# Kernel tuning notes

Hardware: AMD Instinct MI355X
Metric: run time of the kernel (lower is better)

## Reference

```python
import jax, jax.numpy as jnp
import numpy as np

# Static configuration (mirrors init_kwargs)
B, C, H, W = 4, 256, 128, 128
S, T = 512, 64          # style_dim, num style tokens
HC, HS = 4, 8           # cross-attn heads, spatial-attn heads
WS, G = 8, 4            # window size, groupnorm groups
SHARPEN = 2.0
EPS = 1e-5


def _ln(x, g, b):
    m = jnp.mean(x, -1, keepdims=True)
    v = jnp.var(x, -1, keepdims=True)
    return (x - m) * jax.lax.rsqrt(v + EPS) * g + b


def _sdpa(q, k, v, scale):
    # q,k,v: [B, nH, L, D]
    s = jnp.einsum('bhqd,bhkd->bhqk', q, k) * scale
    return jnp.einsum('bhqk,bhkd->bhqd', jax.nn.softmax(s, -1), v)


def _heads(t, nh):
    b, l, c = t.shape
    return t.reshape(b, l, nh, c // nh).transpose(0, 2, 1, 3)


def _unheads(t):
    b, nh, l, d = t.shape
    return t.transpose(0, 2, 1, 3).reshape(b, l, nh * d)


def setup_inputs() -> dict:
    key = jax.random.key(0)
    ks = iter(jax.random.split(key, 48))
    def w(shape, s=0.02):
        return jax.random.normal(next(ks), shape, jnp.float32) * s
    return {
        'x': jax.random.normal(next(ks), (B, C, H, W), jnp.float32),
        'style_code': jax.random.normal(next(ks), (B, S), jnp.float32),
        # SpatialSelfAttention params (1x1 convs == linear over channels)
        'qkv_w': w((3 * C, C)), 'spat_proj_w': w((C, C)),
        # CrossAttnAdaGN params
        'gproj_w': w((2 * C, S)),
        'gproj_b': jnp.concatenate([jnp.ones((C,), jnp.float32), jnp.zeros((C,), jnp.float32)]),
        'tokens_basis': w((T, C)),
        'sproj_w': w((C, S)), 'sproj_b': jnp.zeros((C,), jnp.float32),
        'pos_w1': w((C, 2)), 'pos_b1': jnp.zeros((C,), jnp.float32),
        'pos_w2': w((C, C)), 'pos_b2': jnp.zeros((C,), jnp.float32),
        'q_w': w((C, C)), 'q_b': jnp.zeros((C,), jnp.float32),
        'k_w': w((C, C)), 'k_b': jnp.zeros((C,), jnp.float32),
        'v_w': w((C, C)), 'v_b': jnp.zeros((C,), jnp.float32),
        'o_w': w((C, C)), 'o_b': jnp.zeros((C,), jnp.float32),
        'ffn_w1': w((2 * C, C)), 'ffn_b1': jnp.zeros((2 * C,), jnp.float32),
        'ffn_w2': w((C, 2 * C)), 'ffn_b2': jnp.zeros((C,), jnp.float32),
        'tn_g': jnp.ones((C,), jnp.float32), 'tn_b': jnp.zeros((C,), jnp.float32),
        'qn_g': jnp.ones((C,), jnp.float32), 'qn_b': jnp.zeros((C,), jnp.float32),
        'fn_g': jnp.ones((C,), jnp.float32), 'fn_b': jnp.zeros((C,), jnp.float32),
        'gamma': w((1, C, 1, 1), 0.1),
    }


def reference(x, style_code, qkv_w, spat_proj_w, gproj_w, gproj_b, tokens_basis,
              sproj_w, sproj_b, pos_w1, pos_b1, pos_w2, pos_b2,
              q_w, q_b, k_w, k_b, v_w, v_b, o_w, o_b,
              ffn_w1, ffn_b1, ffn_w2, ffn_b2,
              tn_g, tn_b, qn_g, qn_b, fn_g, fn_b, gamma):
    b = x.shape[0]
    hw = H * W
    # ---------- CrossAttnAdaGN style modulation ----------
    xg = x.reshape(b, G, C // G, H, W)
    mu = jnp.mean(xg, (2, 3, 4), keepdims=True)
    var = jnp.var(xg, (2, 3, 4), keepdims=True)
    normalized = ((xg - mu) * jax.lax.rsqrt(var + EPS)).reshape(b, C, H, W)
    gp = style_code @ gproj_w.T + gproj_b           # [B, 2C]
    scale = gp[:, :C, None, None]
    shift = gp[:, C:, None, None]
    style_tokens = tokens_basis[None] + (style_code @ sproj_w.T + sproj_b)[:, None]  # [B,T,C]
    style_tokens = _ln(style_tokens, tn_g, tn_b)
    gy = jnp.linspace(-1.0, 1.0, H)
    gx = jnp.linspace(-1.0, 1.0, W)
    grid_y, grid_x = jnp.meshgrid(gy, gx, indexing='ij')
    pos = jnp.stack([grid_x, grid_y], -1).reshape(hw, 2)                 # [HW,2]
    pos_emb = jax.nn.silu(pos @ pos_w1.T + pos_b1) @ pos_w2.T + pos_b2   # [HW,C]
    tok = normalized.transpose(0, 2, 3, 1).reshape(b, hw, C)
    q_in = _ln(tok + pos_emb[None], qn_g, qn_b)
    q = _heads(q_in @ q_w.T + q_b, HC)                 # [B,HC,HW,hd]
    k = _heads(style_tokens @ k_w.T + k_b, HC)         # [B,HC,T,hd]
    v = _heads(style_tokens @ v_w.T + v_b, HC)
    hd = C // HC
    sc = _unheads(_sdpa(q, k, v, SHARPEN / jnp.sqrt(jnp.float32(hd))))   # [B,HW,C]
    sc = sc @ o_w.T + o_b
    sc = sc + jax.nn.silu(_ln(sc, fn_g, fn_b) @ ffn_w1.T + ffn_b1) @ ffn_w2.T + ffn_b2
    sc_sp = sc.transpose(0, 2, 1).reshape(b, C, H, W)
    adagn = normalized * scale + shift + sc_sp * gamma
    h = x + adagn  # gate = 1.0, residual style modulation
    # ---------- shifted-window self-attention ----------
    sh = WS // 2
    xr = jnp.roll(h, (-sh, -sh), (2, 3))
    qkv = jnp.einsum('oi,bihw->bohw', qkv_w, xr)
    qs, ks_, vs = jnp.split(qkv, 3, axis=1)
    def win(t):  # [B,C,H,W] -> [B*nWin, WS*WS, C]
        return t.reshape(b, C, H // WS, WS, W // WS, WS).transpose(0, 2, 4, 3, 5, 1).reshape(-1, WS * WS, C)
    hd2 = C // HS
    qh = _heads(win(qs), HS)
    kh = _heads(win(ks_), HS)
    vh = _heads(win(vs), HS)
    out = _unheads(_sdpa(qh, kh, vh, 1.0 / jnp.sqrt(jnp.float32(hd2))))
    out = out.reshape(b, H // WS, W // WS, WS, WS, C).transpose(0, 5, 1, 3, 2, 4).reshape(b, C, H, W)
    out = jnp.roll(out, (sh, sh), (2, 3))
    out = jnp.einsum('oi,bihw->bohw', spat_proj_w, out)
    return h + out
```

## Files before the change

### kernel.cpp

```cpp
#include <hip/hip_runtime.h>
#include <stdint.h>

#define DEV __device__ __forceinline__

typedef unsigned short u16;
typedef unsigned int u32;
typedef __attribute__((ext_vector_type(8))) __bf16 bf16x8;
typedef __attribute__((ext_vector_type(4))) float f32x4;

DEV u16 f2b(float f) {
  u32 u = __float_as_uint(f);
  u32 r = (u + 0x7FFFu + ((u >> 16) & 1u)) >> 16;
  return (u16)r;
}
DEV float b2f(u16 u) { return __uint_as_float(((u32)u) << 16); }
DEV void up2(u32 u, float& a, float& b) {
  a = __uint_as_float(u << 16);
  b = __uint_as_float(u & 0xffff0000u);
}
DEV void up8(uint4 t, float* d) {
  up2(t.x, d[0], d[1]); up2(t.y, d[2], d[3]);
  up2(t.z, d[4], d[5]); up2(t.w, d[6], d[7]);
}
DEV float silu_f(float v) { return v / (1.0f + __expf(-v)); }

DEV float redmax16(float v) {
  v = fmaxf(v, __shfl_xor(v, 1));
  v = fmaxf(v, __shfl_xor(v, 2));
  v = fmaxf(v, __shfl_xor(v, 4));
  v = fmaxf(v, __shfl_xor(v, 8));
  return v;
}
DEV float redsum16(float v) {
  v += __shfl_xor(v, 1);
  v += __shfl_xor(v, 2);
  v += __shfl_xor(v, 4);
  v += __shfl_xor(v, 8);
  return v;
}

DEV int wperm(int p) {
  int y = p >> 7, x = p & 127;
  return ((((y >> 3) << 4) + (x >> 3)) << 6) + ((y & 7) << 3) + (x & 7);
}

DEV void gload16(const u16* g, u16* l) {
  __builtin_amdgcn_global_load_lds(
      (const __attribute__((address_space(1))) uint32_t*)(g),
      (__attribute__((address_space(3))) uint32_t*)(l), 16, 0, 0);
}

struct WConv {
  const float* s0; const float* s1; const float* s2; const float* s3;
  const float* s4; const float* s5; const float* s6;
  u16* d0; u16* d1; u16* d2; u16* d3; u16* d4; u16* d5; u16* d6;
};
__global__ void k_conv_all(WConv wc) {
  int i = blockIdx.x * 256 + threadIdx.x;
  if (i >= 180224) return;
  const float* sp[7] = {wc.s0, wc.s1, wc.s2, wc.s3, wc.s4, wc.s5, wc.s6};
  u16* dp[7] = {wc.d0, wc.d1, wc.d2, wc.d3, wc.d4, wc.d5, wc.d6};
  const int n4[7] = {16384, 16384, 32768, 32768, 49152, 16384, 16384};
  int rem = i, seg = 0;
#pragma unroll
  for (int s = 0; s < 7; ++s) {
    if (rem < n4[s]) { seg = s; break; }
    rem -= n4[s];
  }
  float4 v = ((const float4*)sp[seg])[rem];
  u16 t[4] = {f2b(v.x), f2b(v.y), f2b(v.z), f2b(v.w)};
  *(uint2*)(dp[seg] + (rem << 2)) = *(uint2*)t;
}

DEV void breduce2(float& a, float& b, float* red, int tid) {
#pragma unroll
  for (int off = 32; off > 0; off >>= 1) {
    a += __shfl_down(a, off);
    b += __shfl_down(b, off);
  }
  int lane = tid & 63, wv = tid >> 6;
  if (lane == 0) { red[wv * 2] = a; red[wv * 2 + 1] = b; }
  __syncthreads();
  a = red[0] + red[2] + red[4] + red[6];
  b = red[1] + red[3] + red[5] + red[7];
}

template <int XB>
__global__ void k_gn_partial(const float* __restrict__ x, float* __restrict__ partials,
                             u16* __restrict__ xb) {
  __shared__ float red[8];
  int chunk = blockIdx.x;
  size_t base4 = ((size_t)chunk) << 12;
  const float4* x4 = (const float4*)x;
  float a = 0.f, b = 0.f;
#pragma unroll 4
  for (int i = 0; i < 16; ++i) {
    size_t idx = base4 + (i << 8) + threadIdx.x;
    float4 v = x4[idx];
    a += v.x + v.y + v.z + v.w;
    b += v.x * v.x + v.y * v.y + v.z * v.z + v.w * v.w;
    if (XB) {
      u16 t[4] = {f2b(v.x), f2b(v.y), f2b(v.z), f2b(v.w)};
      *(uint2*)(xb + (idx << 2)) = *(uint2*)t;
    }
  }
  breduce2(a, b, red, threadIdx.x);
  if (threadIdx.x == 0) { partials[chunk * 2] = a; partials[chunk * 2 + 1] = b; }
}

__global__ void k_gn_final(const float* __restrict__ partials, float* __restrict__ stats) {
  int g = blockIdx.x, lane = threadIdx.x;
  float a = partials[(((g << 6) + lane) << 1)];
  float b = partials[(((g << 6) + lane) << 1) + 1];
#pragma unroll
  for (int off = 32; off > 0; off >>= 1) {
    a += __shfl_down(a, off);
    b += __shfl_down(b, off);
  }
  if (lane == 0) {
    float mean = a * (1.f / 1048576.f);
    float var = b * (1.f / 1048576.f) - mean * mean;
    stats[g << 1] = mean;
    stats[(g << 1) + 1] = rsqrtf(var + 1e-5f);
  }
}

__global__ void k_style(const float* __restrict__ sc, const float* __restrict__ gw,
                        const float* __restrict__ gb, const float* __restrict__ sw,
                        const float* __restrict__ sb, float* __restrict__ gp,
                        float* __restrict__ stok) {
  __shared__ float row[512];
  int b = blockIdx.y, part = blockIdx.x, tid = threadIdx.x;
  row[tid] = sc[(b << 9) + tid];
  row[tid + 256] = sc[(b << 9) + tid + 256];
  __syncthreads();
  if (part < 2) {
    int o = (part << 8) + tid;
    float s = gb[o];
    const float* wr = gw + ((size_t)o << 9);
#pragma unroll 8
    for (int j = 0; j < 512; ++j) s += row[j] * wr[j];
    gp[(b << 9) + o] = s;
  } else {
    float s = sb[tid];
    const float* wr = sw + ((size_t)tid << 9);
#pragma unroll 8
    for (int j = 0; j < 512; ++j) s += row[j] * wr[j];
    stok[(b << 8) + tid] = s;
  }
}

__global__ void k_styk(const float* __restrict__ tb, const float* __restrict__ stok,
                       const float* __restrict__ g, const float* __restrict__ bt,
                       float* __restrict__ styk) {
  __shared__ float red[8];
  int r = blockIdx.x;
  int b = r >> 6, t = r & 63;
  int c = threadIdx.x;
  float v = tb[(t << 8) + c] + stok[(b << 8) + c];
  float a = v, bb = v * v;
  breduce2(a, bb, red, c);
  float mean = a * (1.f / 256.f);
  float var = bb * (1.f / 256.f) - mean * mean;
  float rs = rsqrtf(var + 1e-5f);
  styk[((size_t)r << 8) + c] = (v - mean) * rs * g[c] + bt[c];
}

__global__ void k_kv(const float* __restrict__ styk, const float* __restrict__ kw,
                     const float* __restrict__ kb, const float* __restrict__ vw,
                     const float* __restrict__ vb, u16* __restrict__ kmat,
                     u16* __restrict__ vmat) {
  __shared__ float srow[256];
  int r = blockIdx.x, c = threadIdx.x;
  srow[c] = styk[((size_t)r << 8) + c];
  __syncthreads();
  float sk = kb[c], sv = vb[c];
  const float* kr = kw + ((size_t)c << 8);
  const float* vr = vw + ((size_t)c << 8);
#pragma unroll 8
  for (int j = 0; j < 256; ++j) { sk += srow[j] * kr[j]; sv += srow[j] * vr[j]; }
  kmat[((size_t)r << 8) + c] = f2b(sk);
  vmat[((size_t)r << 8) + c] = f2b(sv);
}

__global__ void k_posh(const float* __restrict__ w1, const float* __restrict__ b1,
                       u16* __restrict__ posh) {
  int i = blockIdx.x * 256 + threadIdx.x;
  int stride = gridDim.x * 256;
  for (; i < 16384 * 256; i += stride) {
    int p = i >> 8, c = i & 255;
    int y = p >> 7, x = p & 127;
    float gx = -1.f + 2.f * (float)x / 127.f;
    float gy = -1.f + 2.f * (float)y / 127.f;
    float v = gx * w1[c << 1] + gy * w1[(c << 1) + 1] + b1[c];
    posh[i] = f2b(silu_f(v));
  }
}

template <int ACT, int BIAS, int RES, int SPLIT>
__global__ __launch_bounds__(256, 2) void k_gemm2(
    const u16* __restrict__ A, const u16* __restrict__ Bw,
    const float* __restrict__ bias, const u16* __restrict__ res,
    u16* __restrict__ o0, u16* __restrict__ o1, u16* __restrict__ o2,
    int M, int N, int K) {
  __shared__ __align__(16) u16 lds[17408];
  u16* sA = lds;
  u16* sB = lds + 4096;
  const int tid = threadIdx.x;
  const int lane = tid & 63, wv = tid >> 6;
  const int nx = gridDim.x;
  const int L = blockIdx.x + nx * blockIdx.y;
  const int xcd = L & 7;
  const int t = L >> 3;
  const int nblk = t % nx;
  const int mblk = ((t / nx) << 3) + xcd;
  const int m0 = mblk << 7, n0 = nblk << 7;
  const int l15 = lane & 15, lg = lane >> 4;
  const int wr = wv >> 1, wc = wv & 1;

  const int gofs = (((lane & 3) ^ ((lane >> 3) & 3)) << 3);
  const int lrow = lane >> 2;
  const u16* Ag0 = A + (size_t)(m0 + (wv << 5) + lrow) * K + gofs;
  const u16* Ag1 = A + (size_t)(m0 + (wv << 5) + 16 + lrow) * K + gofs;
  const u16* Bg0 = Bw + (size_t)(n0 + (wv << 5) + lrow) * K + gofs;
  const u16* Bg1 = Bw + (size_t)(n0 + (wv << 5) + 16 + lrow) * K + gofs;
  u16* lA0 = sA + (wv << 10);
  u16* lA1 = sA + (wv << 10) + 512;
  u16* lB0 = sB + (wv << 10);
  u16* lB1 = sB + (wv << 10) + 512;

  const int roff = l15 * 32 + (((lg ^ ((l15 >> 1) & 3))) << 3);
  const int abase = (wr << 6) * 32;
  const int bbase = (wc << 6) * 32;

  f32x4 acc[4][4];
  f32x4 zz = {0.f, 0.f, 0.f, 0.f};
#pragma unroll
  for (int mi = 0; mi < 4; ++mi)
#pragma unroll
    for (int ni = 0; ni < 4; ++ni) acc[mi][ni] = zz;

  for (int kt = 0; kt < K; kt += 32) {
    __syncthreads();
    gload16(Ag0 + kt, lA0);
    gload16(Ag1 + kt, lA1);
    gload16(Bg0 + kt, lB0);
    gload16(Bg1 + kt, lB1);
    __syncthreads();
    bf16x8 af[4], bfv[4];
#pragma unroll
    for (int mi = 0; mi < 4; ++mi) af[mi] = *(const bf16x8*)&sA[abase + mi * 512 + roff];
#pragma unroll
    for (int ni = 0; ni < 4; ++ni) bfv[ni] = *(const bf16x8*)&sB[bbase + ni * 512 + roff];
#pragma unroll
    for (int mi = 0; mi < 4; ++mi)
#pragma unroll
      for (int ni = 0; ni < 4; ++ni)
        acc[mi][ni] = __builtin_amdgcn_mfma_f32_16x16x32_bf16(af[mi], bfv[ni], acc[mi][ni], 0, 0, 0);
  }

  float bv[4];
#pragma unroll
  for (int ni = 0; ni < 4; ++ni)
    bv[ni] = BIAS ? bias[n0 + (wc << 6) + (ni << 4) + l15] : 0.0f;
  __syncthreads();
  const int lg4 = lg << 2;
#pragma unroll
  for (int mi = 0; mi < 4; ++mi) {
#pragma unroll
    for (int ni = 0; ni < 4; ++ni) {
#pragma unroll
      for (int r = 0; r < 4; ++r) {
        int row = (wr << 6) + (mi << 4) + lg4 + r;
        int col = (wc << 6) + (ni << 4) + l15;
        float v = acc[mi][ni][r] + bv[ni];
        if (ACT == 1) v = silu_f(v);
        lds[row * 136 + col] = f2b(v);
      }
    }
  }
  __syncthreads();
  u16* obase;
  int cb, ldc;
  if (SPLIT) {
    int sel = n0 >> 8;
    obase = sel == 0 ? o0 : (sel == 1 ? o1 : o2);
    cb = n0 & 255;
    ldc = 256;
  } else {
    obase = o0;
    cb = n0;
    ldc = N;
  }
#pragma unroll
  for (int i = 0; i < 8; ++i) {
    int flat = (i << 8) + tid;
    int row = flat >> 4, c8 = (flat & 15) << 3;
    uint4 vv = *(const uint4*)&lds[row * 136 + c8];
    size_t oi;
    if (SPLIT) {
      int m = m0 + row;
      int orow = (m & ~16383) | wperm(m & 16383);
      oi = (size_t)orow * 256 + cb + c8;
    } else {
      oi = (size_t)(m0 + row) * ldc + cb + c8;
    }
    if (RES) {
      uint4 rr = *(const uint4*)(res + oi);
      float a8[8], r8[8];
      up8(vv, a8);
      up8(rr, r8);
      u16 t8[8];
#pragma unroll
      for (int e = 0; e < 8; ++e) t8[e] = f2b(a8[e] + r8[e]);
      vv = *(const uint4*)t8;
    }
    *(uint4*)(obase + oi) = vv;
  }
}

template <int XB>
__global__ __launch_bounds__(256) void k_tokpe2(
    const float* __restrict__ x, const u16* __restrict__ xb,
    const float* __restrict__ stats, const u16* __restrict__ pe,
    const float* __restrict__ qg, const float* __restrict__ qb2,
    u16* __restrict__ tokq) {
  __shared__ u16 T[256 * 72];
  __shared__ float red[64][8];
  const int tid = threadIdx.x;
  const int p0 = blockIdx.x << 6, b = blockIdx.y;
  {
    const int c = tid;
    const int g = (b << 2) + (c >> 6);
    const float mu = stats[g << 1], rs = stats[(g << 1) + 1];
    const size_t base = (((size_t)(b << 8) + c) << 14) + p0;
#pragma unroll
    for (int j8 = 0; j8 < 8; ++j8) {
      float f[8];
      if (XB) {
        up8(*(const uint4*)(xb + base + (j8 << 3)), f);
      } else {
        float4 v0 = *(const float4*)(x + base + (j8 << 3));
        float4 v1 = *(const float4*)(x + base + (j8 << 3) + 4);
        f[0] = v0.x; f[1] = v0.y; f[2] = v0.z; f[3] = v0.w;
        f[4] = v1.x; f[5] = v1.y; f[6] = v1.z; f[7] = v1.w;
      }
      u16 t8[8];
#pragma unroll
      for (int e = 0; e < 8; ++e) t8[e] = f2b((f[e] - mu) * rs);
      *(uint4*)&T[c * 72 + (j8 << 3)] = *(uint4*)t8;
    }
  }
  __syncthreads();
  const int p = tid & 63, cq = tid >> 6;
  const size_t pebase = (((size_t)(p0 + p)) << 8) + (cq << 6);
  float vbuf[64];
  float a = 0.f, s = 0.f;
#pragma unroll
  for (int q = 0; q < 8; ++q) {
    float pf[8];
    up8(*(const uint4*)(pe + pebase + (q << 3)), pf);
#pragma unroll
    for (int e = 0; e < 8; ++e) {
      int j = (q << 3) + e;
      float v = b2f(T[((cq << 6) + j) * 72 + p]) + pf[e];
      vbuf[j] = v;
      a += v; s += v * v;
    }
  }
  red[p][cq << 1] = a;
  red[p][(cq << 1) + 1] = s;
  __syncthreads();
  float sa = red[p][0] + red[p][2] + red[p][4] + red[p][6];
  float ss = red[p][1] + red[p][3] + red[p][5] + red[p][7];
  float mean = sa * (1.f / 256.f);
  float var = ss * (1.f / 256.f) - mean * mean;
  float rsg = rsqrtf(var + 1e-5f);
  const size_t orow = (((size_t)(b << 14) + p0 + p) << 8) + (cq << 6);
#pragma unroll
  for (int q = 0; q < 8; ++q) {
    u16 t8[8];
#pragma unroll
    for (int e = 0; e < 8; ++e) {
      int j = (q << 3) + e;
      t8[e] = f2b((vbuf[j] - mean) * rsg * qg[(cq << 6) + j] + qb2[(cq << 6) + j]);
    }
    *(uint4*)(tokq + orow + (q << 3)) = *(uint4*)t8;
  }
}

__global__ __launch_bounds__(256) void k_rowln8(const u16* __restrict__ in,
                                                const float* __restrict__ g,
                                                const float* __restrict__ bt,
                                                u16* __restrict__ out) {
  __shared__ float gs[256], bs[256];
  int tid = threadIdx.x;
  gs[tid] = g[tid];
  bs[tid] = bt[tid];
  __syncthreads();
  size_t base = (((size_t)(blockIdx.x << 5) + (tid >> 3)) << 8) + ((tid & 7) << 5);
  float v[32];
#pragma unroll
  for (int q = 0; q < 4; ++q) up8(*(const uint4*)(in + base + (q << 3)), &v[q << 3]);
  float a = 0.f, b = 0.f;
#pragma unroll
  for (int j = 0; j < 32; ++j) { a += v[j]; b += v[j] * v[j]; }
#pragma unroll
  for (int m = 1; m <= 4; m <<= 1) { a += __shfl_xor(a, m); b += __shfl_xor(b, m); }
  float mean = a * (1.f / 256.f);
  float var = b * (1.f / 256.f) - mean * mean;
  float rs = rsqrtf(var + 1e-5f);
  int c0 = (tid & 7) << 5;
#pragma unroll
  for (int q = 0; q < 4; ++q) {
    u16 tmp[8];
#pragma unroll
    for (int e = 0; e < 8; ++e) {
      int j = (q << 3) + e;
      tmp[e] = f2b((v[j] - mean) * rs * gs[c0 + j] + bs[c0 + j]);
    }
    *(uint4*)(out + base + (q << 3)) = *(uint4*)tmp;
  }
}

__global__ __launch_bounds__(256, 2) void k_cross_mfma(
    const u16* __restrict__ qmat, const u16* __restrict__ kmat,
    const u16* __restrict__ vmat, u16* __restrict__ attn_out) {
  __shared__ u16 Kl[64 * 72];
  __shared__ u16 Vt[64 * 72];
  __shared__ u16 Pl[4][64 * 72];
  const int tid = threadIdx.x;
  const int lane = tid & 63, wv = tid >> 6;
  const int l15 = lane & 15, lg = lane >> 4;
  const int b = blockIdx.z, h = blockIdx.y;
  const int q0 = blockIdx.x << 8;
  for (int c = tid; c < 512; c += 256) {
    int t = c >> 3, dg = (c & 7) << 3;
    size_t src = (((size_t)(b << 6) + t) << 8) + (h << 6) + dg;
    *(uint4*)&Kl[t * 72 + dg] = *(const uint4*)(kmat + src);
    uint4 vv = *(const uint4*)(vmat + src);
    const u16* pv = (const u16*)&vv;
#pragma unroll
    for (int e = 0; e < 8; ++e) Vt[(dg + e) * 72 + t] = pv[e];
  }
  __syncthreads();
  const size_t qrow0 = (size_t)(b << 14) + q0 + (wv << 6);
  f32x4 acc[4][4];
  f32x4 zz = {0.f, 0.f, 0.f, 0.f};
#pragma unroll
  for (int mi = 0; mi < 4; ++mi)
#pragma unroll
    for (int ni = 0; ni < 4; ++ni) acc[mi][ni] = zz;
#pragma unroll
  for (int ks = 0; ks < 2; ++ks) {
    bf16x8 a[4], bbf[4];
#pragma unroll
    for (int mi = 0; mi < 4; ++mi)
      a[mi] = *(const bf16x8*)(qmat + ((qrow0 + (mi << 4) + l15) << 8) + (h << 6) +
                               (ks << 5) + (lg << 3));
#pragma unroll
    for (int ni = 0; ni < 4; ++ni)
      bbf[ni] = *(const bf16x8*)&Kl[((ni << 4) + l15) * 72 + (ks << 5) + (lg << 3)];
#pragma unroll
    for (int mi = 0; mi < 4; ++mi)
#pragma unroll
      for (int ni = 0; ni < 4; ++ni)
        acc[mi][ni] = __builtin_amdgcn_mfma_f32_16x16x32_bf16(a[mi], bbf[ni], acc[mi][ni], 0, 0, 0);
  }
  const float SC = 0.25f;
#pragma unroll
  for (int mi = 0; mi < 4; ++mi) {
#pragma unroll
    for (int r = 0; r < 4; ++r) {
      float rm = acc[mi][0][r];
#pragma unroll
      for (int ni = 1; ni < 4; ++ni) rm = fmaxf(rm, acc[mi][ni][r]);
      rm = redmax16(rm);
      float pv[4];
      float rs = 0.f;
#pragma unroll
      for (int ni = 0; ni < 4; ++ni) {
        pv[ni] = __expf((acc[mi][ni][r] - rm) * SC);
        rs += pv[ni];
      }
      rs = redsum16(rs);
      float inv = 1.f / rs;
      int row = (mi << 4) + (lg << 2) + r;
#pragma unroll
      for (int ni = 0; ni < 4; ++ni)
        Pl[wv][row * 72 + (ni << 4) + l15] = f2b(pv[ni] * inv);
    }
  }
  __syncthreads();
  f32x4 o[4][4];
#pragma unroll
  for (int mi = 0; mi < 4; ++mi)
#pragma unroll
    for (int ni = 0; ni < 4; ++ni) o[mi][ni] = zz;
#pragma unroll
  for (int ks = 0; ks < 2; ++ks) {
    bf16x8 a[4], bbf[4];
#pragma unroll
    for (int mi = 0; mi < 4; ++mi)
      a[mi] = *(const bf16x8*)&Pl[wv][((mi << 4) + l15) * 72 + (ks << 5) + (lg << 3)];
#pragma unroll
    for (int ni = 0; ni < 4; ++ni)
      bbf[ni] = *(const bf16x8*)&Vt[((ni << 4) + l15) * 72 + (ks << 5) + (lg << 3)];
#pragma unroll
    for (int mi = 0; mi < 4; ++mi)
#pragma unroll
      for (int ni = 0; ni < 4; ++ni)
        o[mi][ni] = __builtin_amdgcn_mfma_f32_16x16x32_bf16(a[mi], bbf[ni], o[mi][ni], 0, 0, 0);
  }
  __syncthreads();
#pragma unroll
  for (int mi = 0; mi < 4; ++mi)
#pragma unroll
    for (int ni = 0; ni < 4; ++ni)
#pragma unroll
      for (int r = 0; r < 4; ++r)
        Pl[wv][((mi << 4) + (lg << 2) + r) * 72 + (ni << 4) + l15] = f2b(o[mi][ni][r]);
  __syncthreads();
  const int l8r = lane >> 3, l8c = lane & 7;
#pragma unroll
  for (int it = 0; it < 8; ++it) {
    int row = (it << 3) + l8r;
    uint4 vv = *(const uint4*)&Pl[wv][row * 72 + (l8c << 3)];
    *(uint4*)(attn_out + ((qrow0 + row) << 8) + (h << 6) + (l8c << 3)) = vv;
  }
}

__global__ __launch_bounds__(256, 2) void k_win_mfma(
    const u16* __restrict__ qb, const u16* __restrict__ kbuf,
    const u16* __restrict__ vbuf, u16* __restrict__ wout) {
  __shared__ u16 Vt[4][32 * 72];
  __shared__ u16 Pl[4][64 * 72];
  const int tid = threadIdx.x;
  const int lane = tid & 63, wv = tid >> 6;
  const int l15 = lane & 15, lg = lane >> 4;
  const int win = blockIdx.x, b = blockIdx.y;
  const size_t rowbase = (size_t)(b << 14) + (win << 6);
  const float SC = 0.17677669529663687f;
  f32x4 zz = {0.f, 0.f, 0.f, 0.f};
#pragma unroll 1
  for (int h2 = 0; h2 < 2; ++h2) {
    const int h = (wv << 1) + h2;
    const int co = h << 5;
    {
      const u16* src = vbuf + ((rowbase + lane) << 8) + co;
#pragma unroll
      for (int c = 0; c < 4; ++c) {
        uint4 vv = *(const uint4*)(src + (c << 3));
        const u16* pe = (const u16*)&vv;
#pragma unroll
        for (int e = 0; e < 8; ++e) Vt[wv][((c << 3) + e) * 72 + lane] = pe[e];
      }
    }
    f32x4 acc[4][4];
#pragma unroll
    for (int mi = 0; mi < 4; ++mi)
#pragma unroll
      for (int ni = 0; ni < 4; ++ni) acc[mi][ni] = zz;
    {
      bf16x8 a[4], bbf[4];
#pragma unroll
      for (int mi = 0; mi < 4; ++mi)
        a[mi] = *(const bf16x8*)(qb + ((rowbase + (mi << 4) + l15) << 8) + co + (lg << 3));
#pragma unroll
      for (int ni = 0; ni < 4; ++ni)
        bbf[ni] = *(const bf16x8*)(kbuf + ((rowbase + (ni << 4) + l15) << 8) + co + (lg << 3));
#pragma unroll
      for (int mi = 0; mi < 4; ++mi)
#pragma unroll
        for (int ni = 0; ni < 4; ++ni)
          acc[mi][ni] = __builtin_amdgcn_mfma_f32_16x16x32_bf16(a[mi], bbf[ni], acc[mi][ni], 0, 0, 0);
    }
#pragma unroll
    for (int mi = 0; mi < 4; ++mi) {
#pragma unroll
      for (int r = 0; r < 4; ++r) {
        float rm = acc[mi][0][r];
#pragma unroll
        for (int ni = 1; ni < 4; ++ni) rm = fmaxf(rm, acc[mi][ni][r]);
        rm = redmax16(rm);
        float pv[4];
        float rs = 0.f;
#pragma unroll
        for (int ni = 0; ni < 4; ++ni) {
          pv[ni] = __expf((acc[mi][ni][r] - rm) * SC);
          rs += pv[ni];
        }
        rs = redsum16(rs);
        float inv = 1.f / rs;
        int row = (mi << 4) + (lg << 2) + r;
#pragma unroll
        for (int ni = 0; ni < 4; ++ni)
          Pl[wv][row * 72 + (ni << 4) + l15] = f2b(pv[ni] * inv);
      }
    }
    __syncthreads();
    f32x4 o[4][2];
#pragma unroll
    for (int mi = 0; mi < 4; ++mi)
#pragma unroll
      for (int ni = 0; ni < 2; ++ni) o[mi][ni] = zz;
#pragma unroll
    for (int ks = 0; ks < 2; ++ks) {
      bf16x8 a[4], bbf[2];
#pragma unroll
      for (int mi = 0; mi < 4; ++mi)
        a[mi] = *(const bf16x8*)&Pl[wv][((mi << 4) + l15) * 72 + (ks << 5) + (lg << 3)];
#pragma unroll
      for (int ni = 0; ni < 2; ++ni)
        bbf[ni] = *(const bf16x8*)&Vt[wv][((ni << 4) + l15) * 72 + (ks << 5) + (lg << 3)];
#pragma unroll
      for (int mi = 0; mi < 4; ++mi)
#pragma unroll
        for (int ni = 0; ni < 2; ++ni)
          o[mi][ni] = __builtin_amdgcn_mfma_f32_16x16x32_bf16(a[mi], bbf[ni], o[mi][ni], 0, 0, 0);
    }
    __syncthreads();
#pragma unroll
    for (int mi = 0; mi < 4; ++mi)
#pragma unroll
      for (int ni = 0; ni < 2; ++ni)
#pragma unroll
        for (int r = 0; r < 4; ++r)
          Pl[wv][((mi << 4) + (lg << 2) + r) * 72 + (ni << 4) + l15] = f2b(o[mi][ni][r]);
    __syncthreads();
#pragma unroll
    for (int it = 0; it < 4; ++it) {
      int row = (it << 4) + (lane >> 2);
      int cg = (lane & 3) << 3;
      uint4 vv = *(const uint4*)&Pl[wv][row * 72 + cg];
      *(uint4*)(wout + ((rowbase + row) << 8) + co + cg) = vv;
    }
    __syncthreads();
  }
}

template <int XB>
__global__ void k_xrt(const float* __restrict__ x, const u16* __restrict__ xb,
                      const u16* __restrict__ sc2, const float* __restrict__ stats,
                      const float* __restrict__ gp, const float* __restrict__ gamma,
                      u16* __restrict__ xrt) {
  __shared__ float A[64][33];
  __shared__ float Bt[32][65];
  int p0 = blockIdx.x << 6, c0 = blockIdx.y << 5, b = blockIdx.z;
  int tid = threadIdx.x;
#pragma unroll
  for (int i = 0; i < 8; ++i) {
    int flat = (i << 8) + tid;
    int pi = flat >> 5, ci = flat & 31;
    A[pi][ci] = b2f(sc2[(((size_t)(b << 14) + p0 + pi) << 8) + c0 + ci]);
  }
  __syncthreads();
#pragma unroll
  for (int i = 0; i < 8; ++i) {
    int flat = (i << 8) + tid;
    int cc = flat >> 6, px = flat & 63;
    int cch = c0 + cc;
    int g = (b << 2) + (cch >> 6);
    float mu = stats[g << 1], rs = stats[(g << 1) + 1];
    size_t xi = (((size_t)(b << 8) + cch) << 14) + p0 + px;
    float xv = XB ? b2f(xb[xi]) : x[xi];
    float val = xv + (xv - mu) * rs * gp[(b << 9) + cch] + gp[(b << 9) + 256 + cch] +
                A[px][cc] * gamma[cch];
    Bt[cc][px] = val;
  }
  __syncthreads();
#pragma unroll
  for (int i = 0; i < 8; ++i) {
    int flat = (i << 8) + tid;
    int xi2 = flat >> 5, ci = flat & 31;
    int p = p0 + xi2;
    int yy = p >> 7, xx = p & 127;
    int pr = (((yy + 124) & 127) << 7) + ((xx + 124) & 127);
    xrt[(((size_t)(b << 14) + pr) << 8) + c0 + ci] = f2b(Bt[ci][xi2]);
  }
}

__global__ void k_final2(const u16* __restrict__ xr, const u16* __restrict__ out2,
                         float* __restrict__ dout) {
  __shared__ float L[64][33];
  int bx = blockIdx.x;
  int y = bx >> 1, x0 = (bx & 1) << 6;
  int c0 = blockIdx.y << 5, b = blockIdx.z;
  int tid = threadIdx.x;
#pragma unroll
  for (int i = 0; i < 8; ++i) {
    int flat = (i << 8) + tid;
    int xi = flat >> 5, ci = flat & 31;
    int xx = x0 + xi;
    int pr = (((y + 124) & 127) << 7) + ((xx + 124) & 127);
    size_t ii = (((size_t)(b << 14) + pr) << 8) + c0 + ci;
    size_t ii2 = (((size_t)(b << 14) + wperm(pr)) << 8) + c0 + ci;
    L[xi][ci] = b2f(xr[ii]) + b2f(out2[ii2]);
  }
  __syncthreads();
#pragma unroll
  for (int i = 0; i < 8; ++i) {
    int flat = (i << 8) + tid;
    int cc = flat >> 6, xi2 = flat & 63;
    size_t idx = (((size_t)(b << 8) + c0 + cc) << 14) + (y << 7) + x0 + xi2;
    dout[idx] = L[xi2][cc];
  }
}

extern "C" void kernel_launch(void* const* d_in, const int* in_sizes, int n_in,
                              void* d_out, int out_size, void* d_ws, size_t ws_size,
                              hipStream_t stream) {
  (void)in_sizes; (void)n_in; (void)out_size;
  const float* x = (const float*)d_in[0];
  const float* style = (const float*)d_in[1];
  const float* qkv_w = (const float*)d_in[2];
  const float* spat_w = (const float*)d_in[3];
  const float* gproj_w = (const float*)d_in[4];
  const float* gproj_b = (const float*)d_in[5];
  const float* tokens_basis = (const float*)d_in[6];
  const float* sproj_w = (const float*)d_in[7];
  const float* sproj_b = (const float*)d_in[8];
  const float* pos_w1 = (const float*)d_in[9];
  const float* pos_b1 = (const float*)d_in[10];
  const float* pos_w2 = (const float*)d_in[11];
  const float* pos_b2 = (const float*)d_in[12];
  const float* q_w = (const float*)d_in[13];
  const float* q_b = (const float*)d_in[14];
  const float* k_w = (const float*)d_in[15];
  const float* k_b = (const float*)d_in[16];
  const float* v_w = (const float*)d_in[17];
  const float* v_b = (const float*)d_in[18];
  const float* o_w = (const float*)d_in[19];
  const float* o_b = (const float*)d_in[20];
  const float* ffn_w1 = (const float*)d_in[21];
  const float* ffn_b1 = (const float*)d_in[22];
  const float* ffn_w2 = (const float*)d_in[23];
  const float* ffn_b2 = (const float*)d_in[24];
  const float* tn_g = (const float*)d_in[25];
  const float* tn_b = (const float*)d_in[26];
  const float* qn_g = (const float*)d_in[27];
  const float* qn_b = (const float*)d_in[28];
  const float* fn_g = (const float*)d_in[29];
  const float* fn_b = (const float*)d_in[30];
  const float* gamma = (const float*)d_in[31];
  float* dout = (float*)d_out;

  char* w = (char*)d_ws;
  size_t off = 0;
  auto alloc = [&](size_t sz) {
    char* p = w + off;
    off += (sz + 255) & ~(size_t)255;
    return (void*)p;
  };
  float* partials = (float*)alloc(1024 * 2 * 4);
  float* stats = (float*)alloc(32 * 4);
  float* gp = (float*)alloc(4 * 512 * 4);
  float* stok = (float*)alloc(4 * 256 * 4);
  float* styk = (float*)alloc(4 * 64 * 256 * 4);
  u16* kmat = (u16*)alloc(4 * 64 * 256 * 2);
  u16* vmat = (u16*)alloc(4 * 64 * 256 * 2);
  u16* wb_q = (u16*)alloc(65536 * 2);
  u16* wb_o = (u16*)alloc(65536 * 2);
  u16* wb_w1 = (u16*)alloc(131072 * 2);
  u16* wb_w2 = (u16*)alloc(131072 * 2);
  u16* wb_qkv = (u16*)alloc(196608 * 2);
  u16* wb_sp = (u16*)alloc(65536 * 2);
  u16* wb_p2 = (u16*)alloc(65536 * 2);
  const size_t SLOT = (size_t)65536 * 256 * 2;
  u16* S0 = (u16*)alloc(SLOT);
  u16* S1 = (u16*)alloc(SLOT);
  u16* S2 = (u16*)alloc(SLOT);
  size_t off_base = off;
  u16* xb = (u16*)alloc((size_t)16777216 * 2);
  if (ws_size < off_base) return;
  const int XB = (ws_size >= off) ? 1 : 0;

  u16* ffn_h = (u16*)d_out;
  u16* kwin = (u16*)d_out;
  u16* vwin = (u16*)d_out + (size_t)65536 * 256;

  WConv wc = {q_w, o_w, ffn_w1, ffn_w2, qkv_w, spat_w, pos_w2,
              wb_q, wb_o, wb_w1, wb_w2, wb_qkv, wb_sp, wb_p2};
  k_conv_all<<<704, 256, 0, stream>>>(wc);

  if (XB) k_gn_partial<1><<<1024, 256, 0, stream>>>(x, partials, xb);
  else k_gn_partial<0><<<1024, 256, 0, stream>>>(x, partials, xb);
  k_gn_final<<<16, 64, 0, stream>>>(partials, stats);

  k_style<<<dim3(3, 4), 256, 0, stream>>>(style, gproj_w, gproj_b, sproj_w, sproj_b, gp, stok);
  k_styk<<<256, 256, 0, stream>>>(tokens_basis, stok, tn_g, tn_b, styk);
  k_kv<<<256, 256, 0, stream>>>(styk, k_w, k_b, v_w, v_b, kmat, vmat);

  k_posh<<<4096, 256, 0, stream>>>(pos_w1, pos_b1, S0);
  k_gemm2<0, 1, 0, 0><<<dim3(2, 128), 256, 0, stream>>>(S0, wb_p2, pos_b2, nullptr,
                                                        S1, nullptr, nullptr, 16384, 256, 256);

  if (XB) k_tokpe2<1><<<dim3(256, 4), 256, 0, stream>>>(x, xb, stats, S1, qn_g, qn_b, S2);
  else k_tokpe2<0><<<dim3(256, 4), 256, 0, stream>>>(x, xb, stats, S1, qn_g, qn_b, S2);

  k_gemm2<0, 1, 0, 0><<<dim3(2, 512), 256, 0, stream>>>(S2, wb_q, q_b, nullptr,
                                                        S1, nullptr, nullptr, 65536, 256, 256);
  k_cross_mfma<<<dim3(64, 4, 4), 256, 0, stream>>>(S1, kmat, vmat, S0);
  k_gemm2<0, 1, 0, 0><<<dim3(2, 512), 256, 0, stream>>>(S0, wb_o, o_b, nullptr,
                                                        S2, nullptr, nullptr, 65536, 256, 256);

  k_rowln8<<<2048, 256, 0, stream>>>(S2, fn_g, fn_b, S1);
  k_gemm2<1, 1, 0, 0><<<dim3(4, 512), 256, 0, stream>>>(S1, wb_w1, ffn_b1, nullptr,
                                                        ffn_h, nullptr, nullptr, 65536, 512, 256);
  k_gemm2<0, 1, 1, 0><<<dim3(2, 512), 256, 0, stream>>>(ffn_h, wb_w2, ffn_b2, S2,
                                                        S0, nullptr, nullptr, 65536, 256, 512);

  if (XB) k_xrt<1><<<dim3(256, 8, 4), 256, 0, stream>>>(x, xb, S0, stats, gp, gamma, S1);
  else k_xrt<0><<<dim3(256, 8, 4), 256, 0, stream>>>(x, xb, S0, stats, gp, gamma, S1);

  k_gemm2<0, 0, 0, 1><<<dim3(6, 512), 256, 0, stream>>>(S1, wb_qkv, nullptr, nullptr,
                                                        S2, kwin, vwin, 65536, 768, 256);

  k_win_mfma<<<dim3(256, 4), 256, 0, stream>>>(S2, kwin, vwin, S0);
  k_gemm2<0, 0, 0, 0><<<dim3(2, 512), 256, 0, stream>>>(S0, wb_sp, nullptr, nullptr,
                                                        S2, nullptr, nullptr, 65536, 256, 256);

  k_final2<<<dim3(256, 8, 4), 256, 0, stream>>>(S1, S2, dout);
}
```

Baseline: 426.3 us.

## Shrink attention P staging buffer and defer softmax normalization to output

Both the cross-attention and window-attention kernels now keep the unnormalized exp scores in registers. They stage them to LDS one 32-column k-slice at a time, which cuts the per-wave P buffer from 72 to 40 columns, and apply the 1/rowsum factor to the PV output instead of to the probabilities. The smaller LDS footprint lets launch bounds rise from 2 to 3 blocks per CU, and some syncthreads between output staging and store are removed. The trade-off is higher register pressure from holding acc and inv across the PV loop, a non-unrolled ks loop, and a slight numerical change because unnormalized P is rounded to bf16.

Result: slower. 538.8 us (+26.4%).

```diff
diff --git a/kernel.cpp b/kernel.cpp
--- a/kernel.cpp
+++ b/kernel.cpp
@@ -423,12 +423,12 @@
   }
 }
 
-__global__ __launch_bounds__(256, 2) void k_cross_mfma(
+__global__ __launch_bounds__(256, 3) void k_cross_mfma(
     const u16* __restrict__ qmat, const u16* __restrict__ kmat,
     const u16* __restrict__ vmat, u16* __restrict__ attn_out) {
   __shared__ u16 Kl[64 * 72];
   __shared__ u16 Vt[64 * 72];
-  __shared__ u16 Pl[4][64 * 72];
+  __shared__ u16 Pl[4][64 * 40];
   const int tid = threadIdx.x;
   const int lane = tid & 63, wv = tid >> 6;
   const int l15 = lane & 15, lg = lane >> 4;
@@ -468,6 +468,7 @@
         acc[mi][ni] = __builtin_amdgcn_mfma_f32_16x16x32_bf16(a[mi], bbf[ni], acc[mi][ni], 0, 0, 0);
   }
   const float SC = 0.25f;
+  float inv[4][4];
 #pragma unroll
   for (int mi = 0; mi < 4; ++mi) {
 #pragma unroll
@@ -476,19 +477,15 @@
 #pragma unroll
       for (int ni = 1; ni < 4; ++ni) rm = fmaxf(rm, acc[mi][ni][r]);
       rm = redmax16(rm);
-      float pv[4];
       float rs = 0.f;
 #pragma unroll
       for (int ni = 0; ni < 4; ++ni) {
-        pv[ni] = __expf((acc[mi][ni][r] - rm) * SC);
-        rs += pv[ni];
+        float pv = __expf((acc[mi][ni][r] - rm) * SC);
+        acc[mi][ni][r] = pv;
+        rs += pv;
       }
       rs = redsum16(rs);
-      float inv = 1.f / rs;
-      int row = (mi << 4) + (lg << 2) + r;
-#pragma unroll
-      for (int ni = 0; ni < 4; ++ni)
-        Pl[wv][row * 72 + (ni << 4) + l15] = f2b(pv[ni] * inv);
+      inv[mi][r] = 1.0f / rs;
     }
   }
   __syncthreads();
@@ -497,12 +494,21 @@
   for (int mi = 0; mi < 4; ++mi)
 #pragma unroll
     for (int ni = 0; ni < 4; ++ni) o[mi][ni] = zz;
-#pragma unroll
+#pragma unroll 1
   for (int ks = 0; ks < 2; ++ks) {
+#pragma unroll
+    for (int mi = 0; mi < 4; ++mi)
+#pragma unroll
+      for (int r = 0; r < 4; ++r) {
+        int row = (mi << 4) + (lg << 2) + r;
+#pragma unroll
+        for (int n2 = 0; n2 < 2; ++n2)
+          Pl[wv][row * 40 + (n2 << 4) + l15] = f2b(acc[mi][(ks << 1) + n2][r]);
+      }
     bf16x8 a[4], bbf[4];
 #pragma unroll
     for (int mi = 0; mi < 4; ++mi)
-      a[mi] = *(const bf16x8*)&Pl[wv][((mi << 4) + l15) * 72 + (ks << 5) + (lg << 3)];
+      a[mi] = *(const bf16x8*)&Pl[wv][((mi << 4) + l15) * 40 + (lg << 3)];
 #pragma unroll
     for (int ni = 0; ni < 4; ++ni)
       bbf[ni] = *(const bf16x8*)&Vt[((ni << 4) + l15) * 72 + (ks << 5) + (lg << 3)];
@@ -513,28 +519,31 @@
         o[mi][ni] = __builtin_amdgcn_mfma_f32_16x16x32_bf16(a[mi], bbf[ni], o[mi][ni], 0, 0, 0);
   }
   __syncthreads();
-#pragma unroll
-  for (int mi = 0; mi < 4; ++mi)
-#pragma unroll
-    for (int ni = 0; ni < 4; ++ni)
-#pragma unroll
-      for (int r = 0; r < 4; ++r)
-        Pl[wv][((mi << 4) + (lg << 2) + r) * 72 + (ni << 4) + l15] = f2b(o[mi][ni][r]);
-  __syncthreads();
-  const int l8r = lane >> 3, l8c = lane & 7;
-#pragma unroll
-  for (int it = 0; it < 8; ++it) {
-    int row = (it << 3) + l8r;
-    uint4 vv = *(const uint4*)&Pl[wv][row * 72 + (l8c << 3)];
-    *(uint4*)(attn_out + ((qrow0 + row) << 8) + (h << 6) + (l8c << 3)) = vv;
-  }
-}
-
-__global__ __launch_bounds__(256, 2) void k_win_mfma(
+#pragma unroll 1
+  for (int oh = 0; oh < 2; ++oh) {
+#pragma unroll
+    for (int mi = 0; mi < 4; ++mi)
+#pragma unroll
+      for (int n2 = 0; n2 < 2; ++n2)
+#pragma unroll
+        for (int r = 0; r < 4; ++r)
+          Pl[wv][((mi << 4) + (lg << 2) + r) * 40 + (n2 << 4) + l15] =
+              f2b(o[mi][(oh << 1) + n2][r] * inv[mi][r]);
+#pragma unroll
+    for (int it = 0; it < 4; ++it) {
+      int row = (it << 4) + (lane >> 2);
+      int cg = (lane & 3) << 3;
+      uint4 vv = *(const uint4*)&Pl[wv][row * 40 + cg];
+      *(uint4*)(attn_out + ((qrow0 + row) << 8) + (h << 6) + (oh << 5) + cg) = vv;
+    }
+  }
+}
+
+__global__ __launch_bounds__(256, 3) void k_win_mfma(
     const u16* __restrict__ qb, const u16* __restrict__ kbuf,
     const u16* __restrict__ vbuf, u16* __restrict__ wout) {
   __shared__ u16 Vt[4][32 * 72];
-  __shared__ u16 Pl[4][64 * 72];
+  __shared__ u16 Pl[4][64 * 40];
   const int tid = threadIdx.x;
   const int lane = tid & 63, wv = tid >> 6;
   const int l15 = lane & 15, lg = lane >> 4;
@@ -575,6 +584,7 @@
         for (int ni = 0; ni < 4; ++ni)
           acc[mi][ni] = __builtin_amdgcn_mfma_f32_16x16x32_bf16(a[mi], bbf[ni], acc[mi][ni], 0, 0, 0);
     }
+    float inv[4][4];
 #pragma unroll
     for (int mi = 0; mi < 4; ++mi) {
 #pragma unroll
@@ -583,19 +593,15 @@
 #pragma unroll
         for (int ni = 1; ni < 4; ++ni) rm = fmaxf(rm, acc[mi][ni][r]);
         rm = redmax16(rm);
-        float pv[4];
         float rs = 0.f;
 #pragma unroll
         for (int ni = 0; ni < 4; ++ni) {
-          pv[ni] = __expf((acc[mi][ni][r] - rm) * SC);
-          rs += pv[ni];
+          float pv = __expf((acc[mi][ni][r] - rm) * SC);
+          acc[mi][ni][r] = pv;
+          rs += pv;
         }
         rs = redsum16(rs);
-        float inv = 1.f / rs;
-        int row = (mi << 4) + (lg << 2) + r;
-#pragma unroll
-        for (int ni = 0; ni < 4; ++ni)
-          Pl[wv][row * 72 + (ni << 4) + l15] = f2b(pv[ni] * inv);
+        inv[mi][r] = 1.0f / rs;
       }
     }
     __syncthreads();
@@ -604,12 +610,21 @@
     for (int mi = 0; mi < 4; ++mi)
 #pragma unroll
       for (int ni = 0; ni < 2; ++ni) o[mi][ni] = zz;
-#pragma unroll
+#pragma unroll 1
     for (int ks = 0; ks < 2; ++ks) {
+#pragma unroll
+      for (int mi = 0; mi < 4; ++mi)
+#pragma unroll
+        for (int r = 0; r < 4; ++r) {
+          int row = (mi << 4) + (lg << 2) + r;
+#pragma unroll
+          for (int n2 = 0; n2 < 2; ++n2)
+            Pl[wv][row * 40 + (n2 << 4) + l15] = f2b(acc[mi][(ks << 1) + n2][r]);
+        }
       bf16x8 a[4], bbf[2];
 #pragma unroll
       for (int mi = 0; mi < 4; ++mi)
-        a[mi] = *(const bf16x8*)&Pl[wv][((mi << 4) + l15) * 72 + (ks << 5) + (lg << 3)];
+        a[mi] = *(const bf16x8*)&Pl[wv][((mi << 4) + l15) * 40 + (lg << 3)];
 #pragma unroll
       for (int ni = 0; ni < 2; ++ni)
         bbf[ni] = *(const bf16x8*)&Vt[wv][((ni << 4) + l15) * 72 + (ks << 5) + (lg << 3)];
@@ -626,13 +641,13 @@
       for (int ni = 0; ni < 2; ++ni)
 #pragma unroll
         for (int r = 0; r < 4; ++r)
-          Pl[wv][((mi << 4) + (lg << 2) + r) * 72 + (ni << 4) + l15] = f2b(o[mi][ni][r]);
-    __syncthreads();
+          Pl[wv][((mi << 4) + (lg << 2) + r) * 40 + (ni << 4) + l15] =
+              f2b(o[mi][ni][r] * inv[mi][r]);
 #pragma unroll
     for (int it = 0; it < 4; ++it) {
       int row = (it << 4) + (lane >> 2);
       int cg = (lane & 3) << 3;
-      uint4 vv = *(const uint4*)&Pl[wv][row * 72 + cg];
+      uint4 vv = *(const uint4*)&Pl[wv][row * 40 + cg];
       *(uint4*)(wout + ((rowbase + row) << 8) + co + cg) = vv;
     }
     __syncthreads();
```
